# Kernel optimization log

Measured on AMD Instinct MI355X. Metric: run time of the kernel, lower is better.

The kernel has to match this reference:

```python
import jax, jax.numpy as jnp
import numpy as np

N = 100000
E = 3200000
D = 512

def setup_inputs() -> dict:
    key = jax.random.key(0)
    ks = jax.random.split(key, 6)
    X = jax.random.normal(ks[0], (N, D), dtype=jnp.float32)
    edge_row = jax.random.randint(ks[1], (E,), 0, N, dtype=jnp.int32)
    edge_col = jax.random.randint(ks[2], (E,), 0, N, dtype=jnp.int32)
    edge_val = jax.random.uniform(ks[3], (E,), dtype=jnp.float32)
    # glorot-uniform-ish init for weights
    lim = (6.0 / (D + D)) ** 0.5
    W1 = jax.random.uniform(ks[4], (D, D), dtype=jnp.float32, minval=-lim, maxval=lim)
    W2 = jax.random.uniform(ks[5], (D, D), dtype=jnp.float32, minval=-lim, maxval=lim)
    return {"X": X, "edge_row": edge_row, "edge_col": edge_col,
            "edge_val": edge_val, "W1": W1, "W2": W2}

def _spmm(edge_row, edge_col, edge_val, H):
    # out[r] = sum_{e: row[e]==r} val[e] * H[col[e]]
    msgs = edge_val[:, None] * H[edge_col]          # [E, D]
    return jax.ops.segment_sum(msgs, edge_row, num_segments=N)

def reference(X, edge_row, edge_col, edge_val, W1, W2):
    # layer 1: An @ (X @ W1), tanh activation, no bias
    h = jnp.tanh(_spmm(edge_row, edge_col, edge_val, X @ W1))
    # layer 2
    h = jnp.tanh(_spmm(edge_row, edge_col, edge_val, h @ W2))
    # tf.nn.l2_normalize(curr, axis=1)
    norm = jnp.sqrt(jnp.maximum(jnp.sum(h * h, axis=1, keepdims=True), 1e-12))
    return h / norm
```

## Files before the change

kernel.cpp:

```cpp
#include <hip/hip_runtime.h>
#include <hip/hip_fp16.h>

#define D_DIM 512

typedef __attribute__((ext_vector_type(8))) _Float16 half8;
typedef __attribute__((ext_vector_type(4))) float f32x4;
typedef __attribute__((ext_vector_type(2))) float float2v;

__device__ inline unsigned short f16b(float f) {
  return __half_as_ushort(__float2half(f));
}


__device__ inline void glds16(const _Float16* g, _Float16* l) {
  __builtin_amdgcn_global_load_lds(
      (const __attribute__((address_space(1))) void*)g,
      (__attribute__((address_space(3))) void*)l, 16, 0, 0);
}


__global__ __launch_bounds__(256) void k_hist(const int* __restrict__ row, int* __restrict__ cnt, int E) {
  int i = blockIdx.x * blockDim.x + threadIdx.x;
  if (i < E) atomicAdd(&cnt[row[i]], 1);
}

__global__ __launch_bounds__(1024) void k_scanA(const int* __restrict__ cnt, int* __restrict__ rp,
                                                int* __restrict__ bsum, int n) {
  __shared__ int s[1024];
  int i = blockIdx.x * 1024 + threadIdx.x;
  int v = (i < n) ? cnt[i] : 0;
  s[threadIdx.x] = v;
  __syncthreads();
  for (int off = 1; off < 1024; off <<= 1) {
    int t = (threadIdx.x >= off) ? s[threadIdx.x - off] : 0;
    __syncthreads();
    s[threadIdx.x] += t;
    __syncthreads();
  }
  if (i < n) rp[i] = s[threadIdx.x] - v;
  if (threadIdx.x == 1023) bsum[blockIdx.x] = s[1023];
}

__global__ __launch_bounds__(1024) void k_scanB(int* __restrict__ bsum, int nb) {
  __shared__ int s[1024];
  int v = (threadIdx.x < nb) ? bsum[threadIdx.x] : 0;
  s[threadIdx.x] = v;
  __syncthreads();
  for (int off = 1; off < 1024; off <<= 1) {
    int t = (threadIdx.x >= off) ? s[threadIdx.x - off] : 0;
    __syncthreads();
    s[threadIdx.x] += t;
    __syncthreads();
  }
  if (threadIdx.x < nb) bsum[threadIdx.x] = s[threadIdx.x] - v;
}

__global__ __launch_bounds__(256) void k_scanC(int* __restrict__ rp, const int* __restrict__ bsum, int n, int E) {
  int i = blockIdx.x * 256 + threadIdx.x;
  if (i < n) rp[i] += bsum[i >> 10];
  if (i == 0) rp[n] = E;
}

__global__ __launch_bounds__(256) void k_scatter(const int* __restrict__ row, const int* __restrict__ col,
                                                 const float* __restrict__ val, int* __restrict__ cur,
                                                 int2* __restrict__ edat, int E) {
  int i = blockIdx.x * blockDim.x + threadIdx.x;
  if (i < E) {
    int r = row[i];
    int p = atomicAdd(&cur[r], 1);
    edat[p] = make_int2(col[i], __float_as_int(val[i]));
  }
}


__global__ __launch_bounds__(256) void k_convA(const float* __restrict__ X, unsigned* __restrict__ Xf, int N) {
  __shared__ unsigned lds[4096];
  const int Rg = blockIdx.x;
  const long r0 = (long)Rg * 16;
  const int tid = threadIdx.x;
#pragma unroll
  for (int k = 0; k < 8; ++k) {
    int idx = tid + k * 256;
    int r = idx >> 7;
    int q = idx & 127;
    int c0 = q * 4;
    float4 x = make_float4(0.f, 0.f, 0.f, 0.f);
    long gr = r0 + r;
    if (gr < N) x = ((const float4*)X)[gr * 128 + q];
    unsigned h0 = (unsigned)f16b(x.x) | ((unsigned)f16b(x.y) << 16);
    unsigned h1 = (unsigned)f16b(x.z) | ((unsigned)f16b(x.w) << 16);
    int off = (c0 >> 5) * 512 + ((c0 >> 3) & 3) * 128 + r * 8 + (c0 & 7);
    lds[off >> 1] = h0;
    lds[(off >> 1) + 1] = h1;
  }
  __syncthreads();
  uint4* dst = (uint4*)(Xf + (long)Rg * 4096);
  const uint4* src = (const uint4*)lds;
#pragma unroll
  for (int k = 0; k < 4; ++k) {
    int idx = tid + k * 256;
    dst[idx] = src[idx];
  }
}


__global__ __launch_bounds__(256) void k_repackW(const float* __restrict__ W, _Float16* __restrict__ Wf) {
  int n = blockIdx.x * 256 + threadIdx.x;
  int kg = blockIdx.y;
  half8 v;
#pragma unroll
  for (int j = 0; j < 8; ++j) v[j] = (_Float16)W[(kg * 8 + j) * D_DIM + n];
  const long halfidx = ((long)(kg >> 2) * 32 + (n >> 4)) * 512 + (kg & 3) * 128 + (n & 15) * 8;
  *(half8*)(Wf + halfidx) = v;
}


__global__ __launch_bounds__(256) void k_gemm(const _Float16* __restrict__ A,
                                              const _Float16* __restrict__ B,
                                              _Float16* __restrict__ Cout, int MB) {
  const int id = blockIdx.x;
  const int xcd = id & 7;
  const int sgrid = id >> 3;
  const int panel = (sgrid >> 2) * 8 + xcd;
  if (panel >= MB) return;
  const int nb = sgrid & 3;

  const int tid = threadIdx.x;
  const int lane = tid & 63;
  const int w = tid >> 6;
  const int wr = w >> 1, wc = w & 1;
  const int c = lane & 15, g = lane >> 4;
  const long r0 = (long)panel * 128 + wr * 64;
  const int n0 = nb * 128 + wc * 64;

  __shared__ __align__(16) char smem[32768];
  _Float16* Asl = (_Float16*)smem;
  _Float16* Bsl = (_Float16*)(smem + 16384);

  f32x4 acc[4][4] = {};

  const int f0 = w, f1 = w + 4;
  const long aF0 = ((long)(panel * 8 + f0) * 16) * 512 + lane * 8;
  const long aF1 = ((long)(panel * 8 + f1) * 16) * 512 + lane * 8;
  const long bBase = ((long)nb * 8) * 512 + lane * 8;

  for (int s = 0; s < 8; ++s) {
    const int k5a = 2 * s, k5b = 2 * s + 1;
    glds16(A + aF0 + (long)k5a * 512, Asl + (0 * 8 + f0) * 512);
    glds16(A + aF0 + (long)k5b * 512, Asl + (1 * 8 + f0) * 512);
    glds16(A + aF1 + (long)k5a * 512, Asl + (0 * 8 + f1) * 512);
    glds16(A + aF1 + (long)k5b * 512, Asl + (1 * 8 + f1) * 512);
    glds16(B + bBase + ((long)k5a * 32 + f0) * 512, Bsl + (0 * 8 + f0) * 512);
    glds16(B + bBase + ((long)k5b * 32 + f0) * 512, Bsl + (1 * 8 + f0) * 512);
    glds16(B + bBase + ((long)k5a * 32 + f1) * 512, Bsl + (0 * 8 + f1) * 512);
    glds16(B + bBase + ((long)k5b * 32 + f1) * 512, Bsl + (1 * 8 + f1) * 512);
    __syncthreads();
#pragma unroll
    for (int k5loc = 0; k5loc < 2; ++k5loc) {
      half8 a[4], b[4];
#pragma unroll
      for (int mi = 0; mi < 4; ++mi)
        a[mi] = *(const half8*)(Asl + (k5loc * 8 + wr * 4 + mi) * 512 + lane * 8);
#pragma unroll
      for (int ni = 0; ni < 4; ++ni)
        b[ni] = *(const half8*)(Bsl + (k5loc * 8 + wc * 4 + ni) * 512 + lane * 8);
#pragma unroll
      for (int mi = 0; mi < 4; ++mi)
#pragma unroll
        for (int ni = 0; ni < 4; ++ni)
          acc[mi][ni] = __builtin_amdgcn_mfma_f32_16x16x32_f16(a[mi], b[ni], acc[mi][ni], 0, 0, 0);
    }
    __syncthreads();
  }

  float (*ep)[16][68] = (float (*)[16][68])smem;
#pragma unroll
  for (int m = 0; m < 4; ++m) {
#pragma unroll
    for (int nf = 0; nf < 4; ++nf)
#pragma unroll
      for (int j = 0; j < 4; ++j)
        ep[w][g * 4 + j][nf * 16 + c] = acc[m][nf][j];
    __syncthreads();
    {
      const int row = lane >> 2;
      const int ch = lane & 3;
      float v[16];
#pragma unroll
      for (int q = 0; q < 16; ++q) v[q] = ep[w][row][ch * 16 + q];
      half8 h0, h1;
#pragma unroll
      for (int q = 0; q < 8; ++q) {
        h0[q] = (_Float16)v[q];
        h1[q] = (_Float16)v[8 + q];
      }
      _Float16* dst = Cout + (r0 + m * 16 + row) * D_DIM + n0 + ch * 16;
      *(half8*)dst = h0;
      *(half8*)(dst + 8) = h1;
    }
    __syncthreads();
  }
}


template <int MODE>
__global__ __launch_bounds__(256) void k_spmm(const unsigned short* __restrict__ T, const int* __restrict__ rp,
                                              const int2* __restrict__ edat,
                                              unsigned* __restrict__ Hf, float* __restrict__ out) {
  __shared__ float p[4][D_DIM];
  __shared__ float wss[4];
  const int r = blockIdx.x;
  const int tid = threadIdx.x;
  const int w = tid >> 6, lane = tid & 63;
  const int beg = rp[r], end = rp[r + 1];
  const int cnt = end - beg;
  const int eb = beg + ((cnt * w) >> 2);
  const int ee = beg + ((cnt * (w + 1)) >> 2);

  float acc[8] = {};
  const uint4* Tv = (const uint4*)T;
  for (int e = eb; e < ee; ++e) {
    const int2 ed = edat[e];
    const float v = __int_as_float(ed.y);
    uint4 x = Tv[(long)ed.x * 64 + lane];
    unsigned xs[4] = {x.x, x.y, x.z, x.w};
#pragma unroll
    for (int q = 0; q < 4; ++q) {
      float2 f = __half22float2(__builtin_bit_cast(__half2, xs[q]));
      acc[2 * q] = fmaf(v, f.x, acc[2 * q]);
      acc[2 * q + 1] = fmaf(v, f.y, acc[2 * q + 1]);
    }
  }
  *(float4*)&p[w][lane * 8] = make_float4(acc[0], acc[1], acc[2], acc[3]);
  *(float4*)&p[w][lane * 8 + 4] = make_float4(acc[4], acc[5], acc[6], acc[7]);
  __syncthreads();

  const int c = tid * 2;
  float s0 = p[0][c] + p[1][c] + p[2][c] + p[3][c];
  float s1 = p[0][c + 1] + p[1][c + 1] + p[2][c + 1] + p[3][c + 1];
  s0 = tanhf(s0);
  s1 = tanhf(s1);

  if (MODE == 0) {
    unsigned hv = (unsigned)f16b(s0) | ((unsigned)f16b(s1) << 16);
    const long halfidx = ((long)(r >> 4) * 16 + (c >> 5)) * 512 + ((c >> 3) & 3) * 128 + (r & 15) * 8 + (c & 7);
    __builtin_nontemporal_store(hv, Hf + (halfidx >> 1));
  } else {
    float ss = fmaf(s0, s0, s1 * s1);
#pragma unroll
    for (int off = 1; off < 64; off <<= 1) ss += __shfl_xor(ss, off);
    if (lane == 0) wss[w] = ss;
    __syncthreads();
    const float tot = wss[0] + wss[1] + wss[2] + wss[3];
    const float sc = rsqrtf(fmaxf(tot, 1e-12f));
    float2v o;
    o.x = s0 * sc;
    o.y = s1 * sc;
    __builtin_nontemporal_store(o, (float2v*)out + (long)r * 256 + tid);
  }
}


extern "C" void kernel_launch(void* const* d_in, const int* in_sizes, int n_in,
                              void* d_out, int out_size, void* d_ws, size_t ws_size,
                              hipStream_t stream) {
  const float* X = (const float*)d_in[0];
  const int* erow = (const int*)d_in[1];
  const int* ecol = (const int*)d_in[2];
  const float* evalv = (const float*)d_in[3];
  const float* W1 = (const float*)d_in[4];
  const float* W2 = (const float*)d_in[5];
  const int N = in_sizes[0] / D_DIM;
  const int E = in_sizes[1];
  (void)n_in; (void)out_size; (void)ws_size;

  const int MB = (N + 127) / 128;
  const long Mp = (long)MB * 128;

  char* wsp = (char*)d_ws;
  size_t off = 0;
  auto alloc = [&](size_t bytes) {
    void* p = wsp + off;
    off = (off + bytes + 255) & ~(size_t)255;
    return p;
  };
  unsigned short* T  = (unsigned short*)alloc(Mp * D_DIM * 2);
  unsigned* Af = (unsigned*)alloc(Mp * D_DIM * 2);
  int2* edat  = (int2*)alloc((size_t)E * 8);
  int* rowptr = (int*)alloc((size_t)(N + 1) * 4);
  int* cursor = (int*)alloc((size_t)N * 4);
  int* bsum   = (int*)alloc(1024 * 4);
  _Float16* W1f = (_Float16*)alloc((size_t)D_DIM * D_DIM * 2);
  _Float16* W2f = (_Float16*)alloc((size_t)D_DIM * D_DIM * 2);

  const int nScanBlk = (N + 1023) / 1024;
  const int gemmGrid = 32 * ((MB + 7) / 8);

  hipMemsetAsync(cursor, 0, (size_t)N * 4, stream);
  k_hist<<<dim3((E + 255) / 256), dim3(256), 0, stream>>>(erow, cursor, E);
  k_scanA<<<dim3(nScanBlk), dim3(1024), 0, stream>>>(cursor, rowptr, bsum, N);
  k_scanB<<<dim3(1), dim3(1024), 0, stream>>>(bsum, nScanBlk);
  k_scanC<<<dim3((N + 255) / 256), dim3(256), 0, stream>>>(rowptr, bsum, N, E);
  hipMemcpyAsync(cursor, rowptr, (size_t)N * 4, hipMemcpyDeviceToDevice, stream);
  k_scatter<<<dim3((E + 255) / 256), dim3(256), 0, stream>>>(erow, ecol, evalv, cursor, edat, E);

  k_convA<<<dim3((int)(Mp / 16)), dim3(256), 0, stream>>>(X, Af, N);
  k_repackW<<<dim3(2, 64), dim3(256), 0, stream>>>(W1, W1f);
  k_repackW<<<dim3(2, 64), dim3(256), 0, stream>>>(W2, W2f);

  k_gemm<<<dim3(gemmGrid), dim3(256), 0, stream>>>((const _Float16*)Af, W1f, (_Float16*)T, MB);
  k_spmm<0><<<dim3(N), dim3(256), 0, stream>>>(T, rowptr, edat, Af, nullptr);
  k_gemm<<<dim3(gemmGrid), dim3(256), 0, stream>>>((const _Float16*)Af, W2f, (_Float16*)T, MB);
  k_spmm<1><<<dim3(N), dim3(256), 0, stream>>>(T, rowptr, edat, nullptr, (float*)d_out);
}
```

Baseline: 1.444 ms.

## Horizontally fuse preprocessing kernels and overlap edge scatter with first GEMM

Merges the row histogram, the X-to-fp16 conversion and both weight repacks into one launch, with blocks interleaved by index. It also merges the CSR edge scatter with the first GEMM, giving four of every five blocks to the scatter and keeping an XCD-aware panel mapping for the GEMM blocks. The aim is to cut launch overhead and to overlap latency-bound atomic work with compute-bound MFMA work. The risk is that the two kinds of block compete for CUs and LDS, and the GEMM block scheduling gets less regular.

Result: faster. 1.363 ms (-5.6%).

```diff
diff --git a/kernel.cpp b/kernel.cpp
--- a/kernel.cpp
+++ b/kernel.cpp
@@ -18,11 +18,6 @@
       (__attribute__((address_space(3))) void*)l, 16, 0, 0);
 }
 
-
-__global__ __launch_bounds__(256) void k_hist(const int* __restrict__ row, int* __restrict__ cnt, int E) {
-  int i = blockIdx.x * blockDim.x + threadIdx.x;
-  if (i < E) atomicAdd(&cnt[row[i]], 1);
-}
 
 __global__ __launch_bounds__(1024) void k_scanA(const int* __restrict__ cnt, int* __restrict__ rp,
                                                 int* __restrict__ bsum, int n) {
@@ -61,71 +56,89 @@
   if (i == 0) rp[n] = E;
 }
 
-__global__ __launch_bounds__(256) void k_scatter(const int* __restrict__ row, const int* __restrict__ col,
-                                                 const float* __restrict__ val, int* __restrict__ cur,
-                                                 int2* __restrict__ edat, int E) {
-  int i = blockIdx.x * blockDim.x + threadIdx.x;
-  if (i < E) {
-    int r = row[i];
-    int p = atomicAdd(&cur[r], 1);
-    edat[p] = make_int2(col[i], __float_as_int(val[i]));
-  }
-}
-
-
-__global__ __launch_bounds__(256) void k_convA(const float* __restrict__ X, unsigned* __restrict__ Xf, int N) {
+
+__global__ __launch_bounds__(256) void k_fusedA(const float* __restrict__ X, unsigned* __restrict__ Xf, int N,
+                                                const int* __restrict__ erow, int* __restrict__ cnt, int E,
+                                                const float* __restrict__ W1, _Float16* __restrict__ W1f,
+                                                const float* __restrict__ W2, _Float16* __restrict__ W2f,
+                                                int C ) {
   __shared__ unsigned lds[4096];
-  const int Rg = blockIdx.x;
-  const long r0 = (long)Rg * 16;
+  const int id = blockIdx.x;
   const int tid = threadIdx.x;
-#pragma unroll
-  for (int k = 0; k < 8; ++k) {
-    int idx = tid + k * 256;
-    int r = idx >> 7;
-    int q = idx & 127;
-    int c0 = q * 4;
-    float4 x = make_float4(0.f, 0.f, 0.f, 0.f);
-    long gr = r0 + r;
-    if (gr < N) x = ((const float4*)X)[gr * 128 + q];
-    unsigned h0 = (unsigned)f16b(x.x) | ((unsigned)f16b(x.y) << 16);
-    unsigned h1 = (unsigned)f16b(x.z) | ((unsigned)f16b(x.w) << 16);
-    int off = (c0 >> 5) * 512 + ((c0 >> 3) & 3) * 128 + r * 8 + (c0 & 7);
-    lds[off >> 1] = h0;
-    lds[(off >> 1) + 1] = h1;
-  }
-  __syncthreads();
-  uint4* dst = (uint4*)(Xf + (long)Rg * 4096);
-  const uint4* src = (const uint4*)lds;
-#pragma unroll
-  for (int k = 0; k < 4; ++k) {
-    int idx = tid + k * 256;
-    dst[idx] = src[idx];
-  }
-}
-
-
-__global__ __launch_bounds__(256) void k_repackW(const float* __restrict__ W, _Float16* __restrict__ Wf) {
-  int n = blockIdx.x * 256 + threadIdx.x;
-  int kg = blockIdx.y;
-  half8 v;
-#pragma unroll
-  for (int j = 0; j < 8; ++j) v[j] = (_Float16)W[(kg * 8 + j) * D_DIM + n];
-  const long halfidx = ((long)(kg >> 2) * 32 + (n >> 4)) * 512 + (kg & 3) * 128 + (n & 15) * 8;
-  *(half8*)(Wf + halfidx) = v;
-}
-
-
-__global__ __launch_bounds__(256) void k_gemm(const _Float16* __restrict__ A,
-                                              const _Float16* __restrict__ B,
-                                              _Float16* __restrict__ Cout, int MB) {
+  if (id < 3 * C) {
+    const int rem = id % 3;
+    if (rem == 0) {
+      const int Rg = id / 3;
+      const long r0 = (long)Rg * 16;
+#pragma unroll
+      for (int k = 0; k < 8; ++k) {
+        int idx = tid + k * 256;
+        int r = idx >> 7;
+        int q = idx & 127;
+        int c0 = q * 4;
+        float4 x = make_float4(0.f, 0.f, 0.f, 0.f);
+        long gr = r0 + r;
+        if (gr < N) x = ((const float4*)X)[gr * 128 + q];
+        unsigned h0 = (unsigned)f16b(x.x) | ((unsigned)f16b(x.y) << 16);
+        unsigned h1 = (unsigned)f16b(x.z) | ((unsigned)f16b(x.w) << 16);
+        int off = (c0 >> 5) * 512 + ((c0 >> 3) & 3) * 128 + r * 8 + (c0 & 7);
+        lds[off >> 1] = h0;
+        lds[(off >> 1) + 1] = h1;
+      }
+      __syncthreads();
+      uint4* dst = (uint4*)(Xf + (long)Rg * 4096);
+      const uint4* src = (const uint4*)lds;
+#pragma unroll
+      for (int k = 0; k < 4; ++k) dst[tid + k * 256] = src[tid + k * 256];
+    } else {
+      const int hi = (id / 3) * 2 + rem - 1;
+      const int i = hi * 256 + tid;
+      if (i < E) atomicAdd(&cnt[erow[i]], 1);
+    }
+  } else {
+    const int rb = id - 3 * C;
+    const float* W = (rb < 128) ? W1 : W2;
+    _Float16* Wf = (rb < 128) ? W1f : W2f;
+    const int rb2 = rb & 127;
+    const int kg = rb2 >> 1;
+    const int n = (rb2 & 1) * 256 + tid;
+    half8 v;
+#pragma unroll
+    for (int j = 0; j < 8; ++j) v[j] = (_Float16)W[(kg * 8 + j) * D_DIM + n];
+    const long halfidx = ((long)(kg >> 2) * 32 + (n >> 4)) * 512 + (kg & 3) * 128 + (n & 15) * 8;
+    *(half8*)(Wf + halfidx) = v;
+  }
+}
+
+
+__global__ __launch_bounds__(256) void k_fusedB(const _Float16* __restrict__ A,
+                                                const _Float16* __restrict__ B,
+                                                _Float16* __restrict__ Cout, int MB,
+                                                const int* __restrict__ row, const int* __restrict__ col,
+                                                const float* __restrict__ val, int* __restrict__ cur,
+                                                int2* __restrict__ edat, int E) {
+  __shared__ __align__(16) char smem[32768];
   const int id = blockIdx.x;
-  const int xcd = id & 7;
-  const int sgrid = id >> 3;
-  const int panel = (sgrid >> 2) * 8 + xcd;
+  const int tid = threadIdx.x;
+
+  if (id % 5 != 0) {
+    const int si = (id / 5) * 4 + (id % 5) - 1;
+    const int i = si * 256 + tid;
+    if (i < E) {
+      int r = row[i];
+      int p = atomicAdd(&cur[r], 1);
+      edat[p] = make_int2(col[i], __float_as_int(val[i]));
+    }
+    return;
+  }
+
+  const int gi = id / 5;
+  const int sgrid = gi >> 3;
+  const int vxcd = (5 * gi) & 7;
+  const int panel = (sgrid >> 2) * 8 + vxcd;
   if (panel >= MB) return;
   const int nb = sgrid & 3;
 
-  const int tid = threadIdx.x;
   const int lane = tid & 63;
   const int w = tid >> 6;
   const int wr = w >> 1, wc = w & 1;
@@ -133,7 +146,6 @@
   const long r0 = (long)panel * 128 + wr * 64;
   const int n0 = nb * 128 + wc * 64;
 
-  __shared__ __align__(16) char smem[32768];
   _Float16* Asl = (_Float16*)smem;
   _Float16* Bsl = (_Float16*)(smem + 16384);
 
@@ -183,18 +195,106 @@
         ep[w][g * 4 + j][nf * 16 + c] = acc[m][nf][j];
     __syncthreads();
     {
-      const int row = lane >> 2;
+      const int rw = lane >> 2;
       const int ch = lane & 3;
       float v[16];
 #pragma unroll
-      for (int q = 0; q < 16; ++q) v[q] = ep[w][row][ch * 16 + q];
+      for (int q = 0; q < 16; ++q) v[q] = ep[w][rw][ch * 16 + q];
       half8 h0, h1;
 #pragma unroll
       for (int q = 0; q < 8; ++q) {
         h0[q] = (_Float16)v[q];
         h1[q] = (_Float16)v[8 + q];
       }
-      _Float16* dst = Cout + (r0 + m * 16 + row) * D_DIM + n0 + ch * 16;
+      _Float16* dst = Cout + (r0 + m * 16 + rw) * D_DIM + n0 + ch * 16;
+      *(half8*)dst = h0;
+      *(half8*)(dst + 8) = h1;
+    }
+    __syncthreads();
+  }
+}
+
+
+__global__ __launch_bounds__(256) void k_gemm(const _Float16* __restrict__ A,
+                                              const _Float16* __restrict__ B,
+                                              _Float16* __restrict__ Cout, int MB) {
+  const int id = blockIdx.x;
+  const int xcd = id & 7;
+  const int sgrid = id >> 3;
+  const int panel = (sgrid >> 2) * 8 + xcd;
+  if (panel >= MB) return;
+  const int nb = sgrid & 3;
+
+  const int tid = threadIdx.x;
+  const int lane = tid & 63;
+  const int w = tid >> 6;
+  const int wr = w >> 1, wc = w & 1;
+  const int c = lane & 15, g = lane >> 4;
+  const long r0 = (long)panel * 128 + wr * 64;
+  const int n0 = nb * 128 + wc * 64;
+
+  __shared__ __align__(16) char smem[32768];
+  _Float16* Asl = (_Float16*)smem;
+  _Float16* Bsl = (_Float16*)(smem + 16384);
+
+  f32x4 acc[4][4] = {};
+
+  const int f0 = w, f1 = w + 4;
+  const long aF0 = ((long)(panel * 8 + f0) * 16) * 512 + lane * 8;
+  const long aF1 = ((long)(panel * 8 + f1) * 16) * 512 + lane * 8;
+  const long bBase = ((long)nb * 8) * 512 + lane * 8;
+
+  for (int s = 0; s < 8; ++s) {
+    const int k5a = 2 * s, k5b = 2 * s + 1;
+    glds16(A + aF0 + (long)k5a * 512, Asl + (0 * 8 + f0) * 512);
+    glds16(A + aF0 + (long)k5b * 512, Asl + (1 * 8 + f0) * 512);
+    glds16(A + aF1 + (long)k5a * 512, Asl + (0 * 8 + f1) * 512);
+    glds16(A + aF1 + (long)k5b * 512, Asl + (1 * 8 + f1) * 512);
+    glds16(B + bBase + ((long)k5a * 32 + f0) * 512, Bsl + (0 * 8 + f0) * 512);
+    glds16(B + bBase + ((long)k5b * 32 + f0) * 512, Bsl + (1 * 8 + f0) * 512);
+    glds16(B + bBase + ((long)k5a * 32 + f1) * 512, Bsl + (0 * 8 + f1) * 512);
+    glds16(B + bBase + ((long)k5b * 32 + f1) * 512, Bsl + (1 * 8 + f1) * 512);
+    __syncthreads();
+#pragma unroll
+    for (int k5loc = 0; k5loc < 2; ++k5loc) {
+      half8 a[4], b[4];
+#pragma unroll
+      for (int mi = 0; mi < 4; ++mi)
+        a[mi] = *(const half8*)(Asl + (k5loc * 8 + wr * 4 + mi) * 512 + lane * 8);
+#pragma unroll
+      for (int ni = 0; ni < 4; ++ni)
+        b[ni] = *(const half8*)(Bsl + (k5loc * 8 + wc * 4 + ni) * 512 + lane * 8);
+#pragma unroll
+      for (int mi = 0; mi < 4; ++mi)
+#pragma unroll
+        for (int ni = 0; ni < 4; ++ni)
+          acc[mi][ni] = __builtin_amdgcn_mfma_f32_16x16x32_f16(a[mi], b[ni], acc[mi][ni], 0, 0, 0);
+    }
+    __syncthreads();
+  }
+
+  float (*ep)[16][68] = (float (*)[16][68])smem;
+#pragma unroll
+  for (int m = 0; m < 4; ++m) {
+#pragma unroll
+    for (int nf = 0; nf < 4; ++nf)
+#pragma unroll
+      for (int j = 0; j < 4; ++j)
+        ep[w][g * 4 + j][nf * 16 + c] = acc[m][nf][j];
+    __syncthreads();
+    {
+      const int rw = lane >> 2;
+      const int ch = lane & 3;
+      float v[16];
+#pragma unroll
+      for (int q = 0; q < 16; ++q) v[q] = ep[w][rw][ch * 16 + q];
+      half8 h0, h1;
+#pragma unroll
+      for (int q = 0; q < 8; ++q) {
+        h0[q] = (_Float16)v[q];
+        h1[q] = (_Float16)v[8 + q];
+      }
+      _Float16* dst = Cout + (r0 + m * 16 + rw) * D_DIM + n0 + ch * 16;
       *(half8*)dst = h0;
       *(half8*)(dst + 8) = h1;
     }
@@ -295,20 +395,21 @@
 
   const int nScanBlk = (N + 1023) / 1024;
   const int gemmGrid = 32 * ((MB + 7) / 8);
+  const int convBlocks = (int)(Mp / 16);
+  const int histBlocks = (E + 255) / 256;
 
   hipMemsetAsync(cursor, 0, (size_t)N * 4, stream);
-  k_hist<<<dim3((E + 255) / 256), dim3(256), 0, stream>>>(erow, cursor, E);
+  k_fusedA<<<dim3(3 * convBlocks + 256), dim3(256), 0, stream>>>(
+      X, Af, N, erow, cursor, E, W1, W1f, W2, W2f, convBlocks);
+
   k_scanA<<<dim3(nScanBlk), dim3(1024), 0, stream>>>(cursor, rowptr, bsum, N);
   k_scanB<<<dim3(1), dim3(1024), 0, stream>>>(bsum, nScanBlk);
   k_scanC<<<dim3((N + 255) / 256), dim3(256), 0, stream>>>(rowptr, bsum, N, E);
   hipMemcpyAsync(cursor, rowptr, (size_t)N * 4, hipMemcpyDeviceToDevice, stream);
-  k_scatter<<<dim3((E + 255) / 256), dim3(256), 0, stream>>>(erow, ecol, evalv, cursor, edat, E);
-
-  k_convA<<<dim3((int)(Mp / 16)), dim3(256), 0, stream>>>(X, Af, N);
-  k_repackW<<<dim3(2, 64), dim3(256), 0, stream>>>(W1, W1f);
-  k_repackW<<<dim3(2, 64), dim3(256), 0, stream>>>(W2, W2f);
-
-  k_gemm<<<dim3(gemmGrid), dim3(256), 0, stream>>>((const _Float16*)Af, W1f, (_Float16*)T, MB);
+
+  k_fusedB<<<dim3(5 * gemmGrid), dim3(256), 0, stream>>>(
+      (const _Float16*)Af, W1f, (_Float16*)T, MB, erow, ecol, evalv, cursor, edat, E);
+
   k_spmm<0><<<dim3(N), dim3(256), 0, stream>>>(T, rowptr, edat, Af, nullptr);
   k_gemm<<<dim3(gemmGrid), dim3(256), 0, stream>>>((const _Float16*)Af, W2f, (_Float16*)T, MB);
   k_spmm<1><<<dim3(N), dim3(256), 0, stream>>>(T, rowptr, edat, nullptr, (float*)d_out);
```
